# Optimization experiments

Measured on AMD Instinct MI355X. Metric: run time of the kernel, lower is better.

The kernel has to match this reference:

```python
import jax, jax.numpy as jnp
import numpy as np


def setup_inputs() -> dict:
    key = jax.random.key(0)
    k1, k2 = jax.random.split(key)
    b, c, h, w = 16, 1, 2048, 2048
    alpha = 1.0
    x = jax.random.normal(k1, (b, c, h, w), dtype=jnp.float32)
    # learned filter, initialized exactly like the module: [alpha-0.1, alpha, alpha+0.1]
    filt = jnp.concatenate([
        (alpha - 0.1) * jnp.ones((1, 1, h // 2, w // 2), jnp.float32),
        alpha * jnp.ones((1, 1, h // 2, w // 2), jnp.float32),
        (alpha + 0.1) * jnp.ones((1, 1, h // 2, w // 2), jnp.float32),
    ], axis=1)
    return {"x": x, "filt": filt}


def _haar_forward(x):
    # The torch module uses conv weights repeated over ALL (out,in) channel pairs,
    # so every output channel equals the 2x2 Haar combination of the CHANNEL-SUM.
    ch = x.shape[1]
    xs = jnp.sum(x, axis=1, keepdims=True)  # (b,1,h,w)
    a = xs[:, :, 0::2, 0::2]
    b_ = xs[:, :, 0::2, 1::2]
    c_ = xs[:, :, 1::2, 0::2]
    d = xs[:, :, 1::2, 1::2]
    LL = 0.5 * (a + b_ + c_ + d)
    LH = 0.5 * (a - b_ + c_ - d)   # weight [[.5,-.5],[.5,-.5]]
    HL = 0.5 * (a + b_ - c_ - d)   # weight [[.5,.5],[-.5,-.5]]
    HH = 0.5 * (a - b_ - c_ + d)   # weight [[.5,-.5],[-.5,.5]]
    if ch > 1:
        rep = lambda t: jnp.repeat(t, ch, axis=1)
        LL, LH, HL, HH = rep(LL), rep(LH), rep(HL), rep(HH)
    # module returns (LL, HH, HL, LH)
    return LL, HH, HL, LH


def _haar_inverse(LL, LH, HL, HH):
    bsz, ch, h2, w2 = LL.shape
    a = (LL + LH + HL + HH) * 0.5
    b_ = (LL - LH + HL - HH) * 0.5
    c_ = (LL + LH - HL - HH) * 0.5
    d = (LL - LH - HL + HH) * 0.5
    top = jnp.stack([a, b_], axis=-1).reshape(bsz, ch, h2, 2 * w2)  # even rows
    bot = jnp.stack([c_, d], axis=-1).reshape(bsz, ch, h2, 2 * w2)  # odd rows
    return jnp.stack([top, bot], axis=3).reshape(bsz, ch, 2 * h2, 2 * w2)


def reference(x, filt):
    bsz = x.shape[0]
    # forward unpacks (l_x, LH, HL, HH) from (LL, HH, HL, LH) -> name swap is intentional
    l_x, lh, hl, hh = _haar_forward(x)  # lh is actually HH, hh is actually LH
    h_x = jnp.concatenate([lh, hl, hh], axis=1)  # (b,3,h/2,w/2) since c==1
    filtered = h_x * filt  # broadcast over batch == filter.repeat(b,1,1,1)
    f_lh, f_hl, f_hh = jnp.split(filtered, 3, axis=1)
    return _haar_inverse(l_x, f_lh, f_hl, f_hh)
```

## Files before the change

kernel.cpp:

```cpp
#include <hip/hip_runtime.h>


#define B_    16
#define H_    2048
#define W_    2048
#define H2_   1024
#define W2_   1024

__global__ __launch_bounds__(256) void wavelet_fused_kernel(
    const float* __restrict__ x,
    const float* __restrict__ filt,
    float* __restrict__ out)
{
    const unsigned t = blockIdx.x * blockDim.x + threadIdx.x;

    const unsigned b  = t >> 19;
    const unsigned r  = t & ((1u << 19) - 1u);
    const unsigned i  = r >> 9;
    const unsigned jt = r & 511u;
    const unsigned j0 = jt << 1;

    const long long inOff = (((long long)b * H_) + 2 * i) * W_ + (jt << 2);

    const float4 top = *reinterpret_cast<const float4*>(x + inOff);
    const float4 bot = *reinterpret_cast<const float4*>(x + inOff + W_);

    const long long fOff = (long long)i * W2_ + j0;
    const float2 s0 = *reinterpret_cast<const float2*>(filt + 0 * (H2_ * W2_) + fOff);
    const float2 s1 = *reinterpret_cast<const float2*>(filt + 1 * (H2_ * W2_) + fOff);
    const float2 s2 = *reinterpret_cast<const float2*>(filt + 2 * (H2_ * W2_) + fOff);

    float4 orow0, orow1;
    {
        const float A = top.x, Bv = top.y, C = bot.x, D = bot.y;
        const float P = A + Bv + C + D;
        const float q = s0.x * (A - Bv - C + D);
        const float rr = s1.x * (A + Bv - C - D);
        const float ss = s2.x * (A - Bv + C - D);
        orow0.x = 0.25f * (P + q + rr + ss);
        orow0.y = 0.25f * (P - q + rr - ss);
        orow1.x = 0.25f * (P + q - rr - ss);
        orow1.y = 0.25f * (P - q - rr + ss);
    }
    {
        const float A = top.z, Bv = top.w, C = bot.z, D = bot.w;
        const float P = A + Bv + C + D;
        const float q = s0.y * (A - Bv - C + D);
        const float rr = s1.y * (A + Bv - C - D);
        const float ss = s2.y * (A - Bv + C - D);
        orow0.z = 0.25f * (P + q + rr + ss);
        orow0.w = 0.25f * (P - q + rr - ss);
        orow1.z = 0.25f * (P + q - rr - ss);
        orow1.w = 0.25f * (P - q - rr + ss);
    }

    *reinterpret_cast<float4*>(out + inOff) = orow0;
    *reinterpret_cast<float4*>(out + inOff + W_) = orow1;
}

extern "C" void kernel_launch(void* const* d_in, const int* in_sizes, int n_in,
                              void* d_out, int out_size, void* d_ws, size_t ws_size,
                              hipStream_t stream) {
    const float* x    = (const float*)d_in[0];
    const float* filt = (const float*)d_in[1];
    float* out        = (float*)d_out;

    const unsigned total_threads = B_ * H2_ * (W2_ / 2);
    const unsigned block = 256;
    const unsigned grid = total_threads / block;
    wavelet_fused_kernel<<<grid, block, 0, stream>>>(x, filt, out);
}
```

Before: 111.7 us.

## Interleave batch in block index and widen per-thread work with nontemporal access

After: 116.5 us. 1.04x slower.

```diff
diff --git a/kernel.cpp b/kernel.cpp
--- a/kernel.cpp
+++ b/kernel.cpp
@@ -7,55 +7,68 @@
 #define H2_   1024
 #define W2_   1024
 
+typedef float f32x4 __attribute__((ext_vector_type(4)));
+
+struct Quad { float o00, o01, o10, o11; };
+
+__device__ __forceinline__ Quad haar_block(float A, float Bv, float C, float D,
+                                           float f0, float f1, float f2)
+{
+    const float P = A + Bv + C + D;
+    const float q = f0 * (A - Bv - C + D);
+    const float r = f1 * (A + Bv - C - D);
+    const float s = f2 * (A - Bv + C - D);
+    Quad o;
+    o.o00 = 0.25f * (P + q + r + s);
+    o.o01 = 0.25f * (P - q + r - s);
+    o.o10 = 0.25f * (P + q - r - s);
+    o.o11 = 0.25f * (P - q - r + s);
+    return o;
+}
+
 __global__ __launch_bounds__(256) void wavelet_fused_kernel(
     const float* __restrict__ x,
     const float* __restrict__ filt,
     float* __restrict__ out)
 {
-    const unsigned t = blockIdx.x * blockDim.x + threadIdx.x;
+    const unsigned bid = blockIdx.x;
+    const unsigned b   = bid & 15u;
+    const unsigned sp  = bid >> 4;
 
-    const unsigned b  = t >> 19;
-    const unsigned r  = t & ((1u << 19) - 1u);
-    const unsigned i  = r >> 9;
-    const unsigned jt = r & 511u;
-    const unsigned j0 = jt << 1;
+    const unsigned i  = sp;
+    const unsigned jt = threadIdx.x;
 
-    const long long inOff = (((long long)b * H_) + 2 * i) * W_ + (jt << 2);
+    const long long inOff = (((long long)b * H_) + 2 * i) * W_ + (long long)jt * 8;
 
-    const float4 top = *reinterpret_cast<const float4*>(x + inOff);
-    const float4 bot = *reinterpret_cast<const float4*>(x + inOff + W_);
+    const f32x4* xr0 = reinterpret_cast<const f32x4*>(x + inOff);
+    const f32x4* xr1 = reinterpret_cast<const f32x4*>(x + inOff + W_);
+    const f32x4 t0 = __builtin_nontemporal_load(xr0);
+    const f32x4 t1 = __builtin_nontemporal_load(xr0 + 1);
+    const f32x4 c0 = __builtin_nontemporal_load(xr1);
+    const f32x4 c1 = __builtin_nontemporal_load(xr1 + 1);
 
-    const long long fOff = (long long)i * W2_ + j0;
-    const float2 s0 = *reinterpret_cast<const float2*>(filt + 0 * (H2_ * W2_) + fOff);
-    const float2 s1 = *reinterpret_cast<const float2*>(filt + 1 * (H2_ * W2_) + fOff);
-    const float2 s2 = *reinterpret_cast<const float2*>(filt + 2 * (H2_ * W2_) + fOff);
+    const long long fOff = (long long)i * W2_ + (long long)jt * 4;
+    const f32x4 f0 = *reinterpret_cast<const f32x4*>(filt + 0 * (H2_ * W2_) + fOff);
+    const f32x4 f1 = *reinterpret_cast<const f32x4*>(filt + 1 * (H2_ * W2_) + fOff);
+    const f32x4 f2 = *reinterpret_cast<const f32x4*>(filt + 2 * (H2_ * W2_) + fOff);
 
-    float4 orow0, orow1;
-    {
-        const float A = top.x, Bv = top.y, C = bot.x, D = bot.y;
-        const float P = A + Bv + C + D;
-        const float q = s0.x * (A - Bv - C + D);
-        const float rr = s1.x * (A + Bv - C - D);
-        const float ss = s2.x * (A - Bv + C - D);
-        orow0.x = 0.25f * (P + q + rr + ss);
-        orow0.y = 0.25f * (P - q + rr - ss);
-        orow1.x = 0.25f * (P + q - rr - ss);
-        orow1.y = 0.25f * (P - q - rr + ss);
-    }
-    {
-        const float A = top.z, Bv = top.w, C = bot.z, D = bot.w;
-        const float P = A + Bv + C + D;
-        const float q = s0.y * (A - Bv - C + D);
-        const float rr = s1.y * (A + Bv - C - D);
-        const float ss = s2.y * (A - Bv + C - D);
-        orow0.z = 0.25f * (P + q + rr + ss);
-        orow0.w = 0.25f * (P - q + rr - ss);
-        orow1.z = 0.25f * (P + q - rr - ss);
-        orow1.w = 0.25f * (P - q - rr + ss);
-    }
+    const Quad q0 = haar_block(t0.x, t0.y, c0.x, c0.y, f0.x, f1.x, f2.x);
+    const Quad q1 = haar_block(t0.z, t0.w, c0.z, c0.w, f0.y, f1.y, f2.y);
+    const Quad q2 = haar_block(t1.x, t1.y, c1.x, c1.y, f0.z, f1.z, f2.z);
+    const Quad q3 = haar_block(t1.z, t1.w, c1.z, c1.w, f0.w, f1.w, f2.w);
 
-    *reinterpret_cast<float4*>(out + inOff) = orow0;
-    *reinterpret_cast<float4*>(out + inOff + W_) = orow1;
+    f32x4 o0a, o0b, o1a, o1b;
+    o0a.x = q0.o00; o0a.y = q0.o01; o0a.z = q1.o00; o0a.w = q1.o01;
+    o1a.x = q0.o10; o1a.y = q0.o11; o1a.z = q1.o10; o1a.w = q1.o11;
+    o0b.x = q2.o00; o0b.y = q2.o01; o0b.z = q3.o00; o0b.w = q3.o01;
+    o1b.x = q2.o10; o1b.y = q2.o11; o1b.z = q3.o10; o1b.w = q3.o11;
+
+    f32x4* or0 = reinterpret_cast<f32x4*>(out + inOff);
+    f32x4* or1 = reinterpret_cast<f32x4*>(out + inOff + W_);
+    __builtin_nontemporal_store(o0a, or0);
+    __builtin_nontemporal_store(o0b, or0 + 1);
+    __builtin_nontemporal_store(o1a, or1);
+    __builtin_nontemporal_store(o1b, or1 + 1);
 }
 
 extern "C" void kernel_launch(void* const* d_in, const int* in_sizes, int n_in,
@@ -65,7 +78,7 @@
     const float* filt = (const float*)d_in[1];
     float* out        = (float*)d_out;
 
-    const unsigned total_threads = B_ * H2_ * (W2_ / 2);
+    const unsigned total_threads = B_ * H2_ * (W_ / 8);
     const unsigned block = 256;
     const unsigned grid = total_threads / block;
     wavelet_fused_kernel<<<grid, block, 0, stream>>>(x, filt, out);
```
